# Kernel optimization log

Hardware: AMD Instinct MI355X
Metric: run time of the kernel (lower is better)

Reference implementation:

```python
import jax, jax.numpy as jnp
import numpy as np

B, S, D = 64, 2048, 768


def setup_inputs() -> dict:
    key = jax.random.key(0)
    ks = jax.random.split(key, 7)
    scale = 0.02
    inputs = jax.random.normal(ks[0], (B, S, D), dtype=jnp.float32)
    W1 = jax.random.normal(ks[1], (D, D), dtype=jnp.float32) * scale
    b1 = jnp.zeros((D,), dtype=jnp.float32)
    W2 = jax.random.normal(ks[2], (D, D), dtype=jnp.float32) * scale
    b2 = jnp.zeros((D,), dtype=jnp.float32)
    W3 = jax.random.normal(ks[3], (1, D), dtype=jnp.float32) * scale
    b3 = jnp.zeros((1,), dtype=jnp.float32)
    k = 1024  # int(S * (1 - compression_rate)) with compression_rate = 0.5
    return {"inputs": inputs, "W1": W1, "b1": b1, "W2": W2, "b2": b2,
            "W3": W3, "b3": b3, "k": k}


def select_k(y_soft, k, keep_first_unit=True):
    # Faithful to torch version: clone, force token 0 below the global min
    # (so it is always kept), then rank via double argsort.
    if keep_first_unit:
        y_soft = y_soft.at[:, 0].set(y_soft.min() - 1.0)
    sorted_idx = jnp.argsort(y_soft, axis=-1)          # ascending sort indices
    rank = jnp.argsort(sorted_idx, axis=-1)            # rank of each element
    return rank < k                                    # bool [B, S]


def reference(inputs, W1, b1, W2, b2, W3, b3, k):
    # 3-layer MLP scorer: Linear->ReLU->Linear->ReLU->Linear->Sigmoid
    h = jax.nn.relu(jnp.einsum('bsd,ed->bse', inputs, W1) + b1)
    h = jax.nn.relu(jnp.einsum('bsd,ed->bse', h, W2) + b2)
    y_soft = jax.nn.sigmoid(jnp.einsum('bsd,od->bso', h, W3) + b3)[..., 0]  # [B, S]
    y_hard = select_k(y_soft, k)
    return (y_hard, y_soft)
```

## Files before the change

kernel.cpp:

```cpp
#include <hip/hip_runtime.h>
#include <math.h>


typedef _Float16 f16;
typedef __attribute__((ext_vector_type(8))) _Float16 half8;
typedef __attribute__((ext_vector_type(4))) float f32x4;

#define BM 128
#define BN 128
#define BK 32
#define RS 40
#define INV2048 (1.0f/2048.0f)
#define PLANE (BM * BK)
#define BUFH  (4 * PLANE)

typedef __attribute__((address_space(3))) unsigned lds_u32;
typedef __attribute__((address_space(1))) const unsigned gbl_u32;
#define GLOAD16(g, l) __builtin_amdgcn_global_load_lds((gbl_u32*)(g), (lds_u32*)(l), 16, 0, 0)

union HU { unsigned short u; f16 f; };
static __device__ inline unsigned pack_hl(f16 h, f16 l) {
  HU a, b; a.f = h; b.f = l;
  return (unsigned)a.u | ((unsigned)b.u << 16);
}
static __device__ inline f16 u2h(unsigned short u) { HU c; c.u = u; return c.f; }

#define SPLIT16(x, h0, h1, l0, l1)                                   \
  {                                                                  \
    _Pragma("unroll")                                                \
    for (int e = 0; e < 8; ++e) {                                    \
      f16 ha = (f16)x[e];      float fa = (float)ha;                 \
      f16 hb = (f16)x[8 + e];  float fb = (float)hb;                 \
      h0[e] = ha; l0[e] = (f16)((x[e] - fa) * 2048.0f);              \
      h1[e] = hb; l1[e] = (f16)((x[8 + e] - fb) * 2048.0f);          \
    }                                                                \
  }

__global__ __launch_bounds__(256) void presplit_kernel(
    const float* __restrict__ src, f16* __restrict__ hi,
    f16* __restrict__ lo, int n)
{
  int i = (blockIdx.x * 256 + threadIdx.x) * 8;
  const int stride = gridDim.x * 256 * 8;
  for (; i + 7 < n; i += stride) {
    float4 x0 = *(const float4*)(src + i);
    float4 x1 = *(const float4*)(src + i + 4);
    float xs[8] = {x0.x, x0.y, x0.z, x0.w, x1.x, x1.y, x1.z, x1.w};
    half8 h, l;
#pragma unroll
    for (int e = 0; e < 8; ++e) {
      f16 hv = (f16)xs[e];
      h[e] = hv;
      l[e] = (f16)((xs[e] - (float)hv) * 2048.0f);
    }
    *(half8*)(hi + i) = h;
    *(half8*)(lo + i) = l;
  }
}

template<int FUSE>
__global__ __launch_bounds__(256, 2) void gemm_split_kernel(
    const f16* __restrict__ Ahg, const f16* __restrict__ Alg,
    const f16* __restrict__ Bhg, const f16* __restrict__ Blg,
    const float* __restrict__ bias, const float* __restrict__ w3,
    f16* __restrict__ Oh, f16* __restrict__ Ol,
    float* __restrict__ ylogit, int M, int N, int K)
{
  __shared__ f16 L[2 * BUFH];

  const int nwg = gridDim.x;
  const int cpx = nwg >> 3;
  const int n = ((int)blockIdx.x & 7) * cpx + ((int)blockIdx.x >> 3);
  const int nbn = N / BN;
  const int bn = (n % nbn) * BN;
  const int bm = (n / nbn) * BM;

  const int t = threadIdx.x;
  const int lane = t & 63;
  const int wv = t >> 6;
  const int wm = (wv >> 1) * 64;
  const int wn = (wv & 1) * 64;
  const int i16 = lane & 15;
  const int quad = lane >> 4;
  const int swq = quad ^ ((i16 >> 1) & 3);

  const int srow = lane >> 2;
  const int sch = (lane & 3) ^ ((srow >> 1) & 3);
  const f16* sp;
  if (wv == 0)      sp = Ahg + (size_t)bm * K;
  else if (wv == 1) sp = Alg + (size_t)bm * K;
  else if (wv == 2) sp = Bhg + (size_t)bn * K;
  else              sp = Blg + (size_t)bn * K;
  const f16* sbase = sp + (size_t)srow * K + sch * 8;

  f32x4 acc1[4][4] = {};
  f32x4 acc2[4][4] = {};

#pragma unroll
  for (int j = 0; j < 8; ++j)
    GLOAD16(sbase + (size_t)j * 16 * K, (char*)L + wv * 8192 + j * 1024);
  __syncthreads();

  int cur = 0;
  for (int k0 = 0; k0 < K; k0 += BK) {
    const f16* Lb  = L + cur * BUFH;
    const f16* LAh = Lb;
    const f16* LAl = Lb + PLANE;
    const f16* LBh = Lb + 2 * PLANE;
    const f16* LBl = Lb + 3 * PLANE;

    half8 fah[4], fal[4], fbh[4], fbl[4];
#pragma unroll
    for (int i = 0; i < 4; ++i) {
      const int ao = (wm + i * 16 + i16) * BK + swq * 8;
      const int bo = (wn + i * 16 + i16) * BK + swq * 8;
      fah[i] = *(const half8*)&LAh[ao];
      fal[i] = *(const half8*)&LAl[ao];
      fbh[i] = *(const half8*)&LBh[bo];
      fbl[i] = *(const half8*)&LBl[bo];
    }

    if (k0 + BK < K) {
      char* lwb = (char*)L + (cur ^ 1) * (BUFH * 2) + wv * 8192;
#pragma unroll
      for (int j = 0; j < 8; ++j)
        GLOAD16(sbase + (size_t)j * 16 * K + (k0 + BK), lwb + j * 1024);
    }
    __builtin_amdgcn_sched_barrier(0);

#pragma unroll
    for (int im = 0; im < 4; ++im)
#pragma unroll
      for (int in = 0; in < 4; ++in) {
        acc1[im][in] = __builtin_amdgcn_mfma_f32_16x16x32_f16(
            fah[im], fbh[in], acc1[im][in], 0, 0, 0);
        acc2[im][in] = __builtin_amdgcn_mfma_f32_16x16x32_f16(
            fah[im], fbl[in], acc2[im][in], 0, 0, 0);
        acc2[im][in] = __builtin_amdgcn_mfma_f32_16x16x32_f16(
            fal[im], fbh[in], acc2[im][in], 0, 0, 0);
      }

    __syncthreads();
    cur ^= 1;
  }

  if (FUSE == 0) {
#pragma unroll
    for (int in = 0; in < 4; ++in) {
      const int col = bn + wn + in * 16 + i16;
      const float bv = bias[col];
#pragma unroll
      for (int im = 0; im < 4; ++im)
#pragma unroll
        for (int reg = 0; reg < 4; ++reg) {
          const int row = bm + wm + im * 16 + quad * 4 + reg;
          float v = acc1[im][in][reg] + acc2[im][in][reg] * INV2048 + bv;
          v = v > 0.f ? v : 0.f;
          f16 hv = (f16)v;
          Oh[(size_t)row * N + col] = hv;
          Ol[(size_t)row * N + col] = (f16)((v - (float)hv) * 2048.0f);
        }
    }
  } else {
    float psum[4][4];
#pragma unroll
    for (int im = 0; im < 4; ++im)
#pragma unroll
      for (int reg = 0; reg < 4; ++reg) psum[im][reg] = 0.f;

#pragma unroll
    for (int in = 0; in < 4; ++in) {
      const int col = bn + wn + in * 16 + i16;
      const float bv = bias[col];
      const float wv3 = w3[col];
#pragma unroll
      for (int im = 0; im < 4; ++im)
#pragma unroll
        for (int reg = 0; reg < 4; ++reg) {
          float v = acc1[im][in][reg] + acc2[im][in][reg] * INV2048 + bv;
          v = v > 0.f ? v : 0.f;
          psum[im][reg] = fmaf(v, wv3, psum[im][reg]);
        }
    }
#pragma unroll
    for (int off = 1; off < 16; off <<= 1)
#pragma unroll
      for (int im = 0; im < 4; ++im)
#pragma unroll
        for (int reg = 0; reg < 4; ++reg)
          psum[im][reg] += __shfl_xor(psum[im][reg], off, 64);

    if (i16 == 0) {
#pragma unroll
      for (int im = 0; im < 4; ++im)
#pragma unroll
        for (int reg = 0; reg < 4; ++reg)
          atomicAdd(&ylogit[bm + wm + im * 16 + quad * 4 + reg], psum[im][reg]);
    }
  }
}

__global__ __launch_bounds__(256, 2) void gemm1_fb_kernel(
    const float* __restrict__ A, const float* __restrict__ B,
    const float* __restrict__ bias, unsigned* __restrict__ H1,
    int M, int N, int K)
{
  __shared__ f16 Ah[BM * RS], Al[BM * RS], Bh[BN * RS], Bl[BN * RS];

  const int bn = blockIdx.x * BN;
  const int bm = blockIdx.y * BM;
  const int t = threadIdx.x;
  const int r = t >> 1;
  const int h = t & 1;

  const int lane = t & 63;
  const int wv = t >> 6;
  const int wm = (wv >> 1) * 64;
  const int wn = (wv & 1) * 64;
  const int i16 = lane & 15;
  const int quad = lane >> 4;

  f32x4 acc1[4][4] = {};
  f32x4 acc2[4][4] = {};

  const float* Ag = A + (size_t)(bm + r) * K + h * 16;
  const float* Bg = B + (size_t)(bn + r) * K + h * 16;

  for (int k0 = 0; k0 < K; k0 += BK) {
    float xa[16], xb[16];
    *(float4*)&xa[0]  = *(const float4*)(Ag + k0);
    *(float4*)&xa[4]  = *(const float4*)(Ag + k0 + 4);
    *(float4*)&xa[8]  = *(const float4*)(Ag + k0 + 8);
    *(float4*)&xa[12] = *(const float4*)(Ag + k0 + 12);
    *(float4*)&xb[0]  = *(const float4*)(Bg + k0);
    *(float4*)&xb[4]  = *(const float4*)(Bg + k0 + 4);
    *(float4*)&xb[8]  = *(const float4*)(Bg + k0 + 8);
    *(float4*)&xb[12] = *(const float4*)(Bg + k0 + 12);

    half8 ah0, ah1, al0, al1, bh0, bh1, bl0, bl1;
    SPLIT16(xa, ah0, ah1, al0, al1);
    SPLIT16(xb, bh0, bh1, bl0, bl1);

    __syncthreads();
    const int so = r * RS + h * 16;
    *(half8*)&Ah[so] = ah0; *(half8*)&Ah[so + 8] = ah1;
    *(half8*)&Al[so] = al0; *(half8*)&Al[so + 8] = al1;
    *(half8*)&Bh[so] = bh0; *(half8*)&Bh[so + 8] = bh1;
    *(half8*)&Bl[so] = bl0; *(half8*)&Bl[so + 8] = bl1;
    __syncthreads();

    half8 fah[4], fal[4], fbh[4], fbl[4];
#pragma unroll
    for (int i = 0; i < 4; ++i) {
      const int ao = (wm + i * 16 + i16) * RS + quad * 8;
      const int bo = (wn + i * 16 + i16) * RS + quad * 8;
      fah[i] = *(const half8*)&Ah[ao];
      fal[i] = *(const half8*)&Al[ao];
      fbh[i] = *(const half8*)&Bh[bo];
      fbl[i] = *(const half8*)&Bl[bo];
    }
#pragma unroll
    for (int im = 0; im < 4; ++im)
#pragma unroll
      for (int in = 0; in < 4; ++in) {
        acc1[im][in] = __builtin_amdgcn_mfma_f32_16x16x32_f16(
            fah[im], fbh[in], acc1[im][in], 0, 0, 0);
        acc2[im][in] = __builtin_amdgcn_mfma_f32_16x16x32_f16(
            fah[im], fbl[in], acc2[im][in], 0, 0, 0);
        acc2[im][in] = __builtin_amdgcn_mfma_f32_16x16x32_f16(
            fal[im], fbh[in], acc2[im][in], 0, 0, 0);
      }
  }

#pragma unroll
  for (int in = 0; in < 4; ++in) {
    const int col = bn + wn + in * 16 + i16;
    const float bv = bias[col];
#pragma unroll
    for (int im = 0; im < 4; ++im) {
#pragma unroll
      for (int reg = 0; reg < 4; ++reg) {
        const int row = bm + wm + im * 16 + quad * 4 + reg;
        float v = acc1[im][in][reg] + acc2[im][in][reg] * INV2048 + bv;
        v = v > 0.f ? v : 0.f;
        f16 hv = (f16)v;
        f16 lv = (f16)((v - (float)hv) * 2048.0f);
        H1[(size_t)row * N + col] = pack_hl(hv, lv);
      }
    }
  }
}

__global__ __launch_bounds__(256, 2) void gemm2_fb_kernel(
    const unsigned* __restrict__ A, const float* __restrict__ B,
    const float* __restrict__ bias, const float* __restrict__ w3,
    float* __restrict__ ylogit, int M, int N, int K)
{
  __shared__ f16 Ah[BM * RS], Al[BM * RS], Bh[BN * RS], Bl[BN * RS];

  const int bn = blockIdx.x * BN;
  const int bm = blockIdx.y * BM;
  const int t = threadIdx.x;
  const int r = t >> 1;
  const int h = t & 1;

  const int lane = t & 63;
  const int wv = t >> 6;
  const int wm = (wv >> 1) * 64;
  const int wn = (wv & 1) * 64;
  const int i16 = lane & 15;
  const int quad = lane >> 4;

  f32x4 acc1[4][4] = {};
  f32x4 acc2[4][4] = {};

  const unsigned* Ag = A + (size_t)(bm + r) * K + h * 16;
  const float* Bg = B + (size_t)(bn + r) * K + h * 16;

  for (int k0 = 0; k0 < K; k0 += BK) {
    unsigned ua[16];
    float xb[16];
    *(uint4*)&ua[0]  = *(const uint4*)(Ag + k0);
    *(uint4*)&ua[4]  = *(const uint4*)(Ag + k0 + 4);
    *(uint4*)&ua[8]  = *(const uint4*)(Ag + k0 + 8);
    *(uint4*)&ua[12] = *(const uint4*)(Ag + k0 + 12);
    *(float4*)&xb[0]  = *(const float4*)(Bg + k0);
    *(float4*)&xb[4]  = *(const float4*)(Bg + k0 + 4);
    *(float4*)&xb[8]  = *(const float4*)(Bg + k0 + 8);
    *(float4*)&xb[12] = *(const float4*)(Bg + k0 + 12);

    half8 ah0, ah1, al0, al1, bh0, bh1, bl0, bl1;
#pragma unroll
    for (int e = 0; e < 8; ++e) {
      ah0[e] = u2h((unsigned short)(ua[e] & 0xffffu));
      al0[e] = u2h((unsigned short)(ua[e] >> 16));
      ah1[e] = u2h((unsigned short)(ua[8 + e] & 0xffffu));
      al1[e] = u2h((unsigned short)(ua[8 + e] >> 16));
    }
    SPLIT16(xb, bh0, bh1, bl0, bl1);

    __syncthreads();
    const int so = r * RS + h * 16;
    *(half8*)&Ah[so] = ah0; *(half8*)&Ah[so + 8] = ah1;
    *(half8*)&Al[so] = al0; *(half8*)&Al[so + 8] = al1;
    *(half8*)&Bh[so] = bh0; *(half8*)&Bh[so + 8] = bh1;
    *(half8*)&Bl[so] = bl0; *(half8*)&Bl[so + 8] = bl1;
    __syncthreads();

    half8 fah[4], fal[4], fbh[4], fbl[4];
#pragma unroll
    for (int i = 0; i < 4; ++i) {
      const int ao = (wm + i * 16 + i16) * RS + quad * 8;
      const int bo = (wn + i * 16 + i16) * RS + quad * 8;
      fah[i] = *(const half8*)&Ah[ao];
      fal[i] = *(const half8*)&Al[ao];
      fbh[i] = *(const half8*)&Bh[bo];
      fbl[i] = *(const half8*)&Bl[bo];
    }
#pragma unroll
    for (int im = 0; im < 4; ++im)
#pragma unroll
      for (int in = 0; in < 4; ++in) {
        acc1[im][in] = __builtin_amdgcn_mfma_f32_16x16x32_f16(
            fah[im], fbh[in], acc1[im][in], 0, 0, 0);
        acc2[im][in] = __builtin_amdgcn_mfma_f32_16x16x32_f16(
            fah[im], fbl[in], acc2[im][in], 0, 0, 0);
        acc2[im][in] = __builtin_amdgcn_mfma_f32_16x16x32_f16(
            fal[im], fbh[in], acc2[im][in], 0, 0, 0);
      }
  }

  float psum[4][4];
#pragma unroll
  for (int im = 0; im < 4; ++im)
#pragma unroll
    for (int reg = 0; reg < 4; ++reg) psum[im][reg] = 0.f;

#pragma unroll
  for (int in = 0; in < 4; ++in) {
    const int col = bn + wn + in * 16 + i16;
    const float bv = bias[col];
    const float wv3 = w3[col];
#pragma unroll
    for (int im = 0; im < 4; ++im)
#pragma unroll
      for (int reg = 0; reg < 4; ++reg) {
        float v = acc1[im][in][reg] + acc2[im][in][reg] * INV2048 + bv;
        v = v > 0.f ? v : 0.f;
        psum[im][reg] = fmaf(v, wv3, psum[im][reg]);
      }
  }
#pragma unroll
  for (int off = 1; off < 16; off <<= 1)
#pragma unroll
    for (int im = 0; im < 4; ++im)
#pragma unroll
      for (int reg = 0; reg < 4; ++reg)
        psum[im][reg] += __shfl_xor(psum[im][reg], off, 64);

  if (i16 == 0) {
#pragma unroll
    for (int im = 0; im < 4; ++im)
#pragma unroll
      for (int reg = 0; reg < 4; ++reg)
        atomicAdd(&ylogit[bm + wm + im * 16 + quad * 4 + reg], psum[im][reg]);
  }
}

__global__ void sigmoid_kernel(const float* __restrict__ logit,
                               const float* __restrict__ b3,
                               float* __restrict__ ysoft, int n)
{
  int i = blockIdx.x * blockDim.x + threadIdx.x;
  if (i < n) {
    float x = logit[i] + b3[0];
    ysoft[i] = 1.f / (1.f + expf(-x));
  }
}

__global__ __launch_bounds__(256) void rank_kernel(
    const float* __restrict__ ysoft, float* __restrict__ yhard,
    const int* __restrict__ kptr, int S)
{
  __shared__ float row[2048];
  const int b = blockIdx.x;
  const int part = blockIdx.y;
  const float* y = ysoft + (size_t)b * S;
  float* out = yhard + (size_t)b * S;
  const int kk = *kptr;

  for (int i = threadIdx.x; i < S; i += 256) row[i] = y[i];
  __syncthreads();

  const int j = part * 256 + threadIdx.x;
  if (j >= S) return;
  if (j == 0) { out[0] = 1.0f; return; }
  const float v = row[j];
  int cnt = 1;
  for (int i = 1; i < S; ++i) {
    float u = row[i];
    if (u < v || (u == v && i < j)) ++cnt;
  }
  out[j] = (cnt < kk) ? 1.0f : 0.0f;
}

extern "C" void kernel_launch(void* const* d_in, const int* in_sizes, int n_in,
                              void* d_out, int out_size, void* d_ws, size_t ws_size,
                              hipStream_t stream)
{
  const float* X  = (const float*)d_in[0];
  const float* W1 = (const float*)d_in[1];
  const float* b1 = (const float*)d_in[2];
  const float* W2 = (const float*)d_in[3];
  const float* b2 = (const float*)d_in[4];
  const float* W3 = (const float*)d_in[5];
  const float* b3 = (const float*)d_in[6];
  const int*  kpt = (const int*)d_in[7];

  const int D = 768;
  const int M = in_sizes[0] / D;
  const int S = 2048;
  const int Bb = M / S;

  float* ylogit = (float*)d_out;
  float* yhard  = (float*)d_out;
  float* ysoft  = ((float*)d_out) + M;

  const size_t nX = (size_t)M * D;
  const size_t nW = (size_t)D * D;
  const size_t needA = (4 * nX + 4 * nW) * sizeof(f16);

  dim3 blk(256);

  if (ws_size >= needA) {
    f16* Xh  = (f16*)d_ws;
    f16* Xl  = Xh + nX;
    f16* W1h = Xl + nX;
    f16* W1l = W1h + nW;
    f16* W2h = W1l + nW;
    f16* W2l = W2h + nW;
    f16* H1h = W2l + nW;
    f16* H1l = H1h + nX;

    presplit_kernel<<<dim3(2048), blk, 0, stream>>>(X, Xh, Xl, (int)nX);
    presplit_kernel<<<dim3(288), blk, 0, stream>>>(W1, W1h, W1l, (int)nW);
    presplit_kernel<<<dim3(288), blk, 0, stream>>>(W2, W2h, W2l, (int)nW);
    hipMemsetAsync(ylogit, 0, (size_t)M * sizeof(float), stream);

    dim3 g((D / BN) * (M / BM));
    gemm_split_kernel<0><<<g, blk, 0, stream>>>(
        Xh, Xl, W1h, W1l, b1, nullptr, H1h, H1l, nullptr, M, D, D);
    gemm_split_kernel<1><<<g, blk, 0, stream>>>(
        H1h, H1l, W2h, W2l, b2, W3, nullptr, nullptr, ylogit, M, D, D);
  } else {
    unsigned* H1 = (unsigned*)d_ws;
    hipMemsetAsync(ylogit, 0, (size_t)M * sizeof(float), stream);
    dim3 g(D / BN, M / BM);
    gemm1_fb_kernel<<<g, blk, 0, stream>>>(X, W1, b1, H1, M, D, D);
    gemm2_fb_kernel<<<g, blk, 0, stream>>>(H1, W2, b2, W3, ylogit, M, D, D);
  }

  sigmoid_kernel<<<dim3((M + 255) / 256), blk, 0, stream>>>(ylogit, b3, ysoft, M);
  rank_kernel<<<dim3(Bb, 8), blk, 0, stream>>>(ysoft, yhard, kpt, S);
}
```

Measured before the change: 1.734 ms.

## Prefetch two K-tiles ahead with fine-grained vmcnt waits in GEMM main loop

Restructures the double-buffered GEMM loop so global-to-LDS loads run two tiles ahead instead of one. Explicit vmcnt and lgkmcnt waits plus raw s_barrier calls replace the full __syncthreads. The buffer being overwritten is released right after its fragments reach registers, so the prefetch overlaps the whole MFMA block and hides more load latency. The hand-written waitcnt sequencing is fragile: a wrong count could race on LDS.

```diff
diff --git a/kernel.cpp b/kernel.cpp
--- a/kernel.cpp
+++ b/kernel.cpp
@@ -93,17 +93,26 @@
   else              sp = Blg + (size_t)bn * K;
   const f16* sbase = sp + (size_t)srow * K + sch * 8;
 
+#define STAGE(k0, buf)                                                \
+  {                                                                   \
+    char* lwb_ = (char*)L + (buf) * 32768 + wv * 8192;                \
+    _Pragma("unroll")                                                 \
+    for (int j = 0; j < 8; ++j)                                       \
+      GLOAD16(sbase + (size_t)j * 16 * K + (k0), lwb_ + j * 1024);    \
+  }
+
   f32x4 acc1[4][4] = {};
   f32x4 acc2[4][4] = {};
 
-#pragma unroll
-  for (int j = 0; j < 8; ++j)
-    GLOAD16(sbase + (size_t)j * 16 * K, (char*)L + wv * 8192 + j * 1024);
-  __syncthreads();
-
-  int cur = 0;
-  for (int k0 = 0; k0 < K; k0 += BK) {
-    const f16* Lb  = L + cur * BUFH;
+  STAGE(0, 0);
+  STAGE(BK, 1);
+  asm volatile("s_waitcnt vmcnt(8)" ::: "memory");
+  __builtin_amdgcn_s_barrier();
+
+  const int nt = K / BK;
+  for (int tt = 0; tt < nt; ++tt) {
+    __builtin_amdgcn_sched_barrier(0);
+    const f16* Lb  = L + (tt & 1) * BUFH;
     const f16* LAh = Lb;
     const f16* LAl = Lb + PLANE;
     const f16* LBh = Lb + 2 * PLANE;
@@ -119,13 +128,11 @@
       fbh[i] = *(const half8*)&LBh[bo];
       fbl[i] = *(const half8*)&LBl[bo];
     }
-
-    if (k0 + BK < K) {
-      char* lwb = (char*)L + (cur ^ 1) * (BUFH * 2) + wv * 8192;
-#pragma unroll
-      for (int j = 0; j < 8; ++j)
-        GLOAD16(sbase + (size_t)j * 16 * K + (k0 + BK), lwb + j * 1024);
-    }
+    asm volatile("s_waitcnt lgkmcnt(0)" ::: "memory");
+    __builtin_amdgcn_sched_barrier(0);
+    __builtin_amdgcn_s_barrier();
+
+    if (tt + 2 < nt) STAGE((tt + 2) * BK, tt & 1);
     __builtin_amdgcn_sched_barrier(0);
 
 #pragma unroll
@@ -140,9 +147,13 @@
             fal[im], fbh[in], acc2[im][in], 0, 0, 0);
       }
 
-    __syncthreads();
-    cur ^= 1;
-  }
+    if (tt < nt - 1) {
+      if (tt + 2 < nt) asm volatile("s_waitcnt vmcnt(8)" ::: "memory");
+      else             asm volatile("s_waitcnt vmcnt(0)" ::: "memory");
+      __builtin_amdgcn_s_barrier();
+    }
+  }
+#undef STAGE
 
   if (FUSE == 0) {
 #pragma unroll
```

Result: faster. 1.645 ms (-5.1%).
